# Performance work log

Hardware: AMD Instinct MI355X
Metric: run time of the kernel (lower is better)

## Reference

```python
import jax, jax.numpy as jnp
import numpy as np

B, S, D, H, MEL = 64, 512, 512, 8, 80
HD = D // H  # head dim


def _lstm_cell(x, h, c, w_ih, w_hh, b_ih, b_hh):
    # torch gate order: i, f, g, o
    gates = x @ w_ih.T + h @ w_hh.T + b_ih + b_hh
    i, f, g, o = jnp.split(gates, 4, axis=-1)
    c = jax.nn.sigmoid(f) * c + jax.nn.sigmoid(i) * jnp.tanh(g)
    h = jax.nn.sigmoid(o) * jnp.tanh(c)
    return h, c


def setup_inputs() -> dict:
    key = jax.random.key(0)
    ks = jax.random.split(key, 24)
    s = 0.05
    inp = {"encoder_output": jax.random.normal(ks[0], (B, S, D), jnp.float32)}
    # MultiheadAttention params (torch layout: in_proj [3D, D])
    inp["attn_in_w"] = jax.random.normal(ks[1], (3 * D, D), jnp.float32) * s
    inp["attn_in_b"] = jax.random.normal(ks[2], (3 * D,), jnp.float32) * s
    inp["attn_out_w"] = jax.random.normal(ks[3], (D, D), jnp.float32) * s
    inp["attn_out_b"] = jax.random.normal(ks[4], (D,), jnp.float32) * s
    # LSTM1 (2 layers)
    names = [("l1_w_ih0", (4 * D, D)), ("l1_w_hh0", (4 * D, D)), ("l1_b_ih0", (4 * D,)), ("l1_b_hh0", (4 * D,)),
             ("l1_w_ih1", (4 * D, D)), ("l1_w_hh1", (4 * D, D)), ("l1_b_ih1", (4 * D,)), ("l1_b_hh1", (4 * D,)),
             ("l2_w_ih", (4 * D, D)), ("l2_w_hh", (4 * D, D)), ("l2_b_ih", (4 * D,)), ("l2_b_hh", (4 * D,)),
             ("proj_w", (MEL, D)), ("proj_b", (MEL,))]
    for i, (n, shp) in enumerate(names):
        inp[n] = jax.random.normal(ks[5 + i], shp, jnp.float32) * s
    return inp


def reference(encoder_output, attn_in_w, attn_in_b, attn_out_w, attn_out_b,
              l1_w_ih0, l1_w_hh0, l1_b_ih0, l1_b_hh0,
              l1_w_ih1, l1_w_hh1, l1_b_ih1, l1_b_hh1,
              l2_w_ih, l2_w_hh, l2_b_ih, l2_b_hh, proj_w, proj_b):
    b, s, d = encoder_output.shape
    max_len = s * 5
    wq, wk, wv = jnp.split(attn_in_w, 3, axis=0)
    bq, bk, bv = jnp.split(attn_in_b, 3, axis=0)
    # Precompute K, V over encoder output: [B, S, H, HD]
    K = (encoder_output @ wk.T + bk).reshape(b, s, H, HD)
    V = (encoder_output @ wv.T + bv).reshape(b, s, H, HD)
    scale = 1.0 / np.sqrt(HD)

    def attend(x):  # x: [B, D] single-token query
        q = ((x @ wq.T + bq) * scale).reshape(b, H, HD)
        scores = jnp.einsum('bhd,bshd->bhs', q, K)
        w = jax.nn.softmax(scores, axis=-1)
        ctx = jnp.einsum('bhs,bshd->bhd', w, V).reshape(b, d)
        return ctx @ attn_out_w.T + attn_out_b

    zeros = jnp.zeros((b, d), encoder_output.dtype)
    carry0 = (zeros, zeros, zeros, zeros, zeros, zeros, zeros)

    def step(carry, _):
        h10, c10, h11, c11, h2, c2, dec_in = carry
        h10, c10 = _lstm_cell(dec_in, h10, c10, l1_w_ih0, l1_w_hh0, l1_b_ih0, l1_b_hh0)
        h11, c11 = _lstm_cell(h10, h11, c11, l1_w_ih1, l1_w_hh1, l1_b_ih1, l1_b_hh1)
        attn_out = attend(h11)
        h2, c2 = _lstm_cell(attn_out, h2, c2, l2_w_ih, l2_w_hh, l2_b_ih, l2_b_hh)
        out = h2 @ proj_w.T + proj_b  # [B, MEL]
        return (h10, c10, h11, c11, h2, c2, h2), out

    _, ys = jax.lax.scan(step, carry0, None, length=max_len)
    return jnp.transpose(ys, (1, 0, 2))  # [B, max_len, MEL]
```

## Files before the change

kernel.cpp:

```cpp
#include <hip/hip_runtime.h>
#include <hip/hip_bf16.h>
#include <hip/hip_fp8.h>

#define DEV_INLINE __device__ __forceinline__

typedef __attribute__((ext_vector_type(8))) short bf16x8;
typedef __attribute__((ext_vector_type(4))) float f32x4;
typedef __attribute__((ext_vector_type(2))) float f32x2;
typedef __attribute__((ext_vector_type(4))) unsigned int u32x4;
typedef unsigned long long ull;

constexpr int Bc = 64, Sc = 512, Dc = 512, Hc = 8, HDc = 64, MELc = 80, Tc = 2560;
constexpr int OUTSTRIDE = Tc * MELc;

constexpr size_t SZ_KP8 = 64ull * 8 * 512 * 64;
constexpr size_t SZ_VP  = 64ull * 8 * 512 * 64 * 2;
constexpr size_t SZ_PL  = 128ull * 2048 * 16;
constexpr size_t OFF_KP8 = 0;
constexpr size_t OFF_VP  = OFF_KP8 + SZ_KP8;
constexpr size_t OFF_PL0 = OFF_VP + SZ_VP;
constexpr size_t OFF_PL1 = OFF_PL0 + SZ_PL;
constexpr size_t OFF_PL2 = OFF_PL1 + SZ_PL;
constexpr size_t OFF_PWQ = OFF_PL2 + SZ_PL;
constexpr size_t OFF_PP  = OFF_PWQ + 524288;
constexpr size_t OFF_BL0 = OFF_PP + 81920;
constexpr size_t OFF_BL1 = OFF_BL0 + 8192;
constexpr size_t OFF_BL2 = OFF_BL1 + 8192;
constexpr size_t OFF_B2E = OFF_BL2 + 8192;
constexpr size_t OFF_W2E = OFF_B2E + 8192;
constexpr size_t OFF_WOT = OFF_W2E + 2097152;
constexpr size_t OFF_ACT = OFF_WOT + 1048576;
constexpr size_t OFF_FLG = OFF_ACT + 524288;

constexpr unsigned DYN_LDS = 121088;

DEV_INLINE float bf2f(short s) { return __uint_as_float(((unsigned)(unsigned short)s) << 16); }
DEV_INLINE short f2bf(float f) { union { __hip_bfloat16 h; short s; } u; u.h = __float2bfloat16(f); return u.s; }
DEV_INLINE float sig_f(float x) { return 1.0f / (1.0f + __expf(-x)); }
DEV_INLINE float tanh_f(float x) {
  float ax = fabsf(x);
  float e = __expf(fminf(2.0f * ax, 80.0f));
  float r = 1.0f - 2.0f / (e + 1.0f);
  return copysignf(r, x);
}
DEV_INLINE bf16x8 cvt8(const float* p) {
  bf16x8 r;
#pragma unroll
  for (int i = 0; i < 8; ++i) r[i] = f2bf(p[i]);
  return r;
}
DEV_INLINE float fp8tof(unsigned v) {
  __hip_fp8_e4m3 t; t.__x = (__hip_fp8_storage_t)v; return (float)t;
}

template <bool HI>
DEV_INLINE f32x2 cvt2_fp8(unsigned w) {
#if defined(__has_builtin) && __has_builtin(__builtin_amdgcn_cvt_pk_f32_fp8)
  return __builtin_amdgcn_cvt_pk_f32_fp8(w, HI);
#else
  unsigned b = HI ? (w >> 16) : w;
  f32x2 r; r[0] = fp8tof(b & 0xFFu); r[1] = fp8tof((b >> 8) & 0xFFu);
  return r;
#endif
}

DEV_INLINE ull ld_dev_u64(const void* p) {
  return __hip_atomic_load((const ull*)p, __ATOMIC_RELAXED, __HIP_MEMORY_SCOPE_AGENT);
}
DEV_INLINE void st_dev_u64(void* p, ull v) {
  __hip_atomic_store((ull*)p, v, __ATOMIC_RELAXED, __HIP_MEMORY_SCOPE_AGENT);
}
DEV_INLINE bf16x8 ld_frag(const __hip_bfloat16* p) {
  union { bf16x8 v; ull u[2]; } r;
  r.u[0] = ld_dev_u64(p);
  r.u[1] = ld_dev_u64((const char*)p + 8);
  return r.v;
}

__global__ __launch_bounds__(256) void gemm_setup(const float* __restrict__ A,
                                                  const float* __restrict__ Bt,
                                                  const float* __restrict__ bias,
                                                  __hip_bfloat16* __restrict__ dst,
                                                  unsigned char* __restrict__ dst8,
                                                  int mode) {
  int tid = threadIdx.x, lane = tid & 63, wv = tid >> 6;
  int m0 = blockIdx.y * 64 + wv * 16;
  int nb = blockIdx.x * 64;
  int mrow = m0 + (lane & 15);
  int kb = (lane >> 4) * 8;
  f32x4 acc0 = {0,0,0,0}, acc1 = {0,0,0,0}, acc2 = {0,0,0,0}, acc3 = {0,0,0,0};
  const float* arow = A + (size_t)mrow * 512 + kb;
  const float* b0r = Bt + (size_t)(nb + 0 * 16 + (lane & 15)) * 512 + kb;
  const float* b1r = Bt + (size_t)(nb + 1 * 16 + (lane & 15)) * 512 + kb;
  const float* b2r = Bt + (size_t)(nb + 2 * 16 + (lane & 15)) * 512 + kb;
  const float* b3r = Bt + (size_t)(nb + 3 * 16 + (lane & 15)) * 512 + kb;
  for (int kk = 0; kk < 16; ++kk) {
    bf16x8 af = cvt8(arow + kk * 32);
    acc0 = __builtin_amdgcn_mfma_f32_16x16x32_bf16(af, cvt8(b0r + kk * 32), acc0, 0, 0, 0);
    acc1 = __builtin_amdgcn_mfma_f32_16x16x32_bf16(af, cvt8(b1r + kk * 32), acc1, 0, 0, 0);
    acc2 = __builtin_amdgcn_mfma_f32_16x16x32_bf16(af, cvt8(b2r + kk * 32), acc2, 0, 0, 0);
    acc3 = __builtin_amdgcn_mfma_f32_16x16x32_bf16(af, cvt8(b3r + kk * 32), acc3, 0, 0, 0);
  }
  int col16 = lane & 15, r0 = (lane >> 4) * 4;
  f32x4 accs[4] = {acc0, acc1, acc2, acc3};
#pragma unroll
  for (int nt = 0; nt < 4; ++nt) {
    int n = nb + nt * 16 + col16;
#pragma unroll
    for (int r = 0; r < 4; ++r) {
      int m = m0 + r0 + r;
      float v = accs[nt][r];
      if (mode == 0) {
        v += bias[n];
        int bb = m >> 9, s = m & 511, h = n >> 6, d = n & 63;
        dst[(((size_t)(bb * 8 + h) * 512 + s) * 64) + d] = __float2bfloat16(v);
      } else if (mode == 2) {
        v += bias[n];
        int bb = m >> 9, s = m & 511, h = n >> 6, d = n & 63;
        __hip_fp8_e4m3 q(v);
        dst8[(((size_t)(bb * 8 + h) * 512 + s) * 64) + d] = (unsigned char)q.__x;
      } else {
        dst[(size_t)m * 512 + n] = __float2bfloat16(v);
      }
    }
  }
}

__global__ __launch_bounds__(256) void transpose512(const float* __restrict__ in, float* __restrict__ out) {
  __shared__ float tl[32][33];
  int x = threadIdx.x & 31, ty = threadIdx.x >> 5;
  int bx = blockIdx.x * 32, by = blockIdx.y * 32;
#pragma unroll
  for (int r = 0; r < 4; ++r) tl[ty + r * 8][x] = in[(size_t)(by + ty + r * 8) * 512 + bx + x];
  __syncthreads();
#pragma unroll
  for (int r = 0; r < 4; ++r) out[(size_t)(bx + ty + r * 8) * 512 + by + x] = tl[x][ty + r * 8];
}

__global__ __launch_bounds__(256) void b2eff_k(const float* __restrict__ w2ih, const float* __restrict__ bout,
                                               const float* __restrict__ bih, const float* __restrict__ bhh,
                                               float* __restrict__ dst) {
  int g = blockIdx.x * 256 + threadIdx.x;
  float acc = bih[g] + bhh[g];
  const float* row = w2ih + (size_t)g * 512;
  for (int k = 0; k < 512; ++k) acc += row[k] * bout[k];
  dst[g] = acc;
}

__global__ __launch_bounds__(256) void pack_lstm(const float* __restrict__ lo_f32,
                                                 const __hip_bfloat16* __restrict__ lo_bf16,
                                                 const float* __restrict__ hi_f32,
                                                 const float* __restrict__ b1, const float* __restrict__ b2,
                                                 const float* __restrict__ b_pre,
                                                 __hip_bfloat16* __restrict__ dst, float* __restrict__ bias_out,
                                                 int mode) {
  int u = blockIdx.x, tid = threadIdx.x;
  for (int rep = 0; rep < 8; ++rep) {
    int slot = rep * 256 + tid;
    int kk = slot >> 6, lane = slot & 63;
    int n16 = lane & 15, gate = n16 >> 2, jj = n16 & 3;
    int srow = gate * 512 + u * 4 + jj;
    int k = kk * 32 + (lane >> 4) * 8;
    __hip_bfloat16 tmp[8];
    if (k < 512) {
      if (mode == 0) {
#pragma unroll
        for (int i = 0; i < 8; ++i) tmp[i] = __float2bfloat16(lo_f32[(size_t)srow * 512 + k + i]);
      } else {
#pragma unroll
        for (int i = 0; i < 8; ++i) tmp[i] = lo_bf16[(size_t)srow * 512 + k + i];
      }
    } else {
#pragma unroll
      for (int i = 0; i < 8; ++i) tmp[i] = __float2bfloat16(hi_f32[(size_t)srow * 512 + (k - 512) + i]);
    }
    *(uint4*)(dst + ((size_t)u * 2048 + slot) * 8) = *(uint4*)tmp;
  }
  if (tid < 16) {
    int gate = tid >> 2, jj = tid & 3;
    int srow = gate * 512 + u * 4 + jj;
    bias_out[u * 16 + tid] = (mode == 0) ? (b1[srow] + b2[srow]) : b_pre[srow];
  }
}

__global__ __launch_bounds__(256) void pack_wq(const float* __restrict__ wq, __hip_bfloat16* __restrict__ dst) {
  int h = blockIdx.x, tid = threadIdx.x;
  for (int rep = 0; rep < 16; ++rep) {
    int slot = rep * 256 + tid;
    int nt = slot >> 10, kk = (slot >> 6) & 15, lane = slot & 63;
    int srow = h * 64 + nt * 16 + (lane & 15);
    int k = kk * 32 + (lane >> 4) * 8;
    __hip_bfloat16 tmp[8];
#pragma unroll
    for (int i = 0; i < 8; ++i) tmp[i] = __float2bfloat16(wq[(size_t)srow * 512 + k + i]);
    *(uint4*)(dst + ((size_t)h * 4096 + slot) * 8) = *(uint4*)tmp;
  }
}

struct DecParams {
  const float* attn_in_b;
  const float* proj_b;
  const float* proj_w;
  const uint4* packL0; const uint4* packL1; const uint4* packL2;
  const float* biasL0; const float* biasL1; const float* biasL2;
  const uint4* packWq;
  const unsigned char* Kp8; const __hip_bfloat16* Vp;
  __hip_bfloat16* h10b; __hip_bfloat16* h11b; __hip_bfloat16* h2b; __hip_bfloat16* ctxb;
  ull* actbase;
  unsigned* flags;
  float* out;
};

constexpr ull WD_TICKS = 200000000ull;

DEV_INLINE void publish_flag(unsigned* flags, int wg, unsigned id, int tid) {
  __builtin_amdgcn_s_waitcnt(0);
  __syncthreads();
  if (tid == 0)
    __hip_atomic_store(&flags[wg], id, __ATOMIC_RELAXED, __HIP_MEMORY_SCOPE_AGENT);
}

DEV_INLINE bool wait_flags(unsigned* flags, int base, int count, unsigned id, int tid,
                           ull t0, int* bail) {
  if (tid < 64) {
    for (;;) {
      bool ok = true;
      for (int i = tid; i < count; i += 64)
        ok &= (__hip_atomic_load(&flags[base + i], __ATOMIC_RELAXED, __HIP_MEMORY_SCOPE_AGENT) >= id);
      if (__all(ok ? 1 : 0)) break;
      if (__builtin_amdgcn_s_memrealtime() - t0 > WD_TICKS) { if (tid == 0) *bail = 1; break; }
      __builtin_amdgcn_s_sleep(1);
    }
  }
  __syncthreads();
  if (*bail) return false;
  return true;
}

DEV_INLINE bool wait_half(unsigned* flags, int base, unsigned id, int lane, ull t0, int* sbail) {
  for (;;) {
    unsigned f0 = __hip_atomic_load(&flags[base + lane], __ATOMIC_RELAXED, __HIP_MEMORY_SCOPE_AGENT);
    unsigned f1 = __hip_atomic_load(&flags[base + lane], __ATOMIC_RELAXED, __HIP_MEMORY_SCOPE_AGENT);
    if (__all(f0 >= id ? 1 : 0)) return true;
    if (__all(f1 >= id ? 1 : 0)) return true;
    if (__builtin_amdgcn_s_memrealtime() - t0 > WD_TICKS) { *sbail = 1; return false; }
    __builtin_amdgcn_s_sleep(1);
  }
}

DEV_INLINE void prefetch_hi(bf16x8* pf, const __hip_bfloat16* hi, int g, int lane, int wv) {
  if (wv >= 2) {
    const __hip_bfloat16* p = hi + (size_t)(g * 32 + (wv & 1) * 16 + (lane & 15)) * 512 + (lane >> 4) * 8;
#pragma unroll
    for (int kk = 0; kk < 16; ++kk) pf[kk] = ld_frag(p + kk * 32);
  }
}

DEV_INLINE bool lstm_stage(int tid, int g, int wgl,
                           const uint4* wlds, const float* bias,
                           const __hip_bfloat16* lo, const bf16x8* pf,
                           float* cstate, __hip_bfloat16* hc,
                           float* pred, ull* st64,
                           unsigned* flags, int fbase, unsigned id,
                           ull t0, int* sbail) {
  const int lane = tid & 63, wv = tid >> 6, mt = wv & 1, kh = wv >> 1;
  f32x4 acc = {0,0,0,0};
  if (kh == 0) {
    const __hip_bfloat16* pA = lo + (size_t)(g * 32 + mt * 16 + (lane & 15)) * 512 + (lane >> 4) * 8;
    if (wait_half(flags, fbase, id, lane, t0, sbail)) {
#pragma unroll
      for (int kk = 0; kk < 8; ++kk) {
        bf16x8 a = ld_frag(pA + kk * 32);
        bf16x8 b = *(const bf16x8*)(wlds + kk * 64 + lane);
        acc = __builtin_amdgcn_mfma_f32_16x16x32_bf16(a, b, acc, 0, 0, 0);
      }
      if (wait_half(flags, fbase + 64, id, lane, t0, sbail)) {
#pragma unroll
        for (int kk = 8; kk < 16; ++kk) {
          bf16x8 a = ld_frag(pA + kk * 32);
          bf16x8 b = *(const bf16x8*)(wlds + kk * 64 + lane);
          acc = __builtin_amdgcn_mfma_f32_16x16x32_bf16(a, b, acc, 0, 0, 0);
        }
      }
    }
  } else {
#pragma unroll
    for (int kk = 0; kk < 16; ++kk) {
      bf16x8 b = *(const bf16x8*)(wlds + (16 + kk) * 64 + lane);
      acc = __builtin_amdgcn_mfma_f32_16x16x32_bf16(pf[kk], b, acc, 0, 0, 0);
    }
  }
#pragma unroll
  for (int r = 0; r < 4; ++r) pred[wv * 256 + lane * 4 + r] = acc[r];
  __syncthreads();
  if (*sbail) return false;
  if (tid < 128) {
    int bl = tid >> 2, j = tid & 3;
    int mt2 = bl >> 4, qd = (bl & 15) >> 2, reg = bl & 3;
    const float* p0 = pred + mt2 * 256;
    const float* p1 = pred + (2 + mt2) * 256;
    int l0 = qd * 16;
    float gi = p0[(l0 + j) * 4 + reg]      + p1[(l0 + j) * 4 + reg]      + bias[j];
    float gf = p0[(l0 + 4 + j) * 4 + reg]  + p1[(l0 + 4 + j) * 4 + reg]  + bias[4 + j];
    float gg = p0[(l0 + 8 + j) * 4 + reg]  + p1[(l0 + 8 + j) * 4 + reg]  + bias[8 + j];
    float go = p0[(l0 + 12 + j) * 4 + reg] + p1[(l0 + 12 + j) * 4 + reg] + bias[12 + j];
    float c = cstate[tid & 127];
    c = sig_f(gf) * c + sig_f(gi) * tanh_f(gg);
    float h = sig_f(go) * tanh_f(c);
    cstate[tid & 127] = c;
    ((unsigned short*)st64)[tid] = (unsigned short)f2bf(h);
  }
  __syncthreads();
  if (tid < 32)
    st_dev_u64(hc + (size_t)(g * 32 + tid) * 512 + wgl * 4, st64[tid]);
  return true;
}

DEV_INLINE void proj_spread(int tid, int g, int wgl, const float* pw, const float* pb,
                            const __hip_bfloat16* h2in, float* outp) {
  const int lane = tid & 63, pr = tid >> 6;
#pragma unroll
  for (int r = 0; r < 5; ++r) {
    int P = wgl * 20 + r * 4 + pr;
    int b = P / 80, m = P - b * 80;
    bf16x8 hv = ld_frag(h2in + (size_t)(g * 32 + b) * 512 + lane * 8);
    const f32x4* w4 = (const f32x4*)(pw + (size_t)m * 512 + lane * 8);
    f32x4 wa = w4[0], wb = w4[1];
    float acc = bf2f(hv[0]) * wa[0] + bf2f(hv[1]) * wa[1] + bf2f(hv[2]) * wa[2] + bf2f(hv[3]) * wa[3]
              + bf2f(hv[4]) * wb[0] + bf2f(hv[5]) * wb[1] + bf2f(hv[6]) * wb[2] + bf2f(hv[7]) * wb[3];
#pragma unroll
    for (int off = 32; off; off >>= 1) acc += __shfl_xor(acc, off);
    if (lane == 0) outp[(size_t)(g * 32 + b) * OUTSTRIDE + m] = acc + pb[m];
  }
}

__global__ __launch_bounds__(256, 1) void decoder_main(DecParams P) {
  extern __shared__ char smem[];
  uint4* wL0 = (uint4*)smem;
  uint4* wL1 = wL0 + 2048;
  uint4* wL2 = wL1 + 2048;
  ull*   st64 = (ull*)(wL2 + 2048);
  float* pred = (float*)(st64 + 32);
  float* qls  = pred + 1024;
  float* sco  = qls + 1088;
  float* red  = sco + 1024;
  float* cst  = red + 2048;
  float* smx  = cst + 384;
  float* ssum = smx + 4;
  float* sinv = ssum + 4;
  int*   sbail = (int*)(sinv + 2);

  const int wg = blockIdx.x, tid = threadIdx.x;
  const int lane = tid & 63, wv = tid >> 6;
  const int g = wg >> 7;
  const int wgl = wg & 127;
  const int fbase = g * 128;
  const int hh = wgl >> 4;
  const int b0g = (wgl & 15) * 2;
  const int bblk = b0g & ~15;

  const ull t0 = __builtin_amdgcn_s_memrealtime();

  {
    const uint4* s0 = P.packL0 + (size_t)wgl * 2048;
    const uint4* s1 = P.packL1 + (size_t)wgl * 2048;
    const uint4* s2 = P.packL2 + (size_t)wgl * 2048;
    for (int i = tid; i < 2048; i += 256) { wL0[i] = s0[i]; wL1[i] = s1[i]; wL2[i] = s2[i]; }
  }
  if (tid == 0) *sbail = 0;
  if (tid < 128) { cst[tid] = 0.0f; cst[128 + tid] = 0.0f; cst[256 + tid] = 0.0f; }
  st_dev_u64(P.actbase + (size_t)wg * 256 + tid, 0ull);
  __syncthreads();
  publish_flag(P.flags, wg, 1u, tid);
  if (!wait_flags(P.flags, 0, 256, 1u, tid, t0, sbail)) goto bail;

  for (int t = 0; t < Tc; ++t) {
    const int cur = t & 1, pv = cur ^ 1;
    const unsigned idA = 4u * t + 1, idApub = 4u * t + 2, idBpub = 4u * t + 3,
                   idCpub = 4u * t + 4, idDpub = 4u * t + 5;
    __hip_bfloat16* h10c = P.h10b + cur * 32768; __hip_bfloat16* h10p = P.h10b + pv * 32768;
    __hip_bfloat16* h11c = P.h11b + cur * 32768; __hip_bfloat16* h11p = P.h11b + pv * 32768;
    __hip_bfloat16* h2c  = P.h2b  + cur * 32768; __hip_bfloat16* h2p  = P.h2b  + pv * 32768;
    __hip_bfloat16* ctxc = P.ctxb + cur * 32768;

    {
      bf16x8 pf[16];
      prefetch_hi(pf, h10p, g, lane, wv);
      if (!lstm_stage(tid, g, wgl, wL0, P.biasL0 + wgl * 16, h2p, pf, cst, h10c, pred, st64,
                      P.flags, fbase, idA, t0, sbail)) goto bail;
      publish_flag(P.flags, wg, idApub, tid);
    }
    if (t > 0)
      proj_spread(tid, g, wgl, P.proj_w, P.proj_b, h2p, P.out + (size_t)(t - 1) * MELc);

    {
      bf16x8 pf[16];
      prefetch_hi(pf, h11p, g, lane, wv);
      if (!lstm_stage(tid, g, wgl, wL1, P.biasL1 + wgl * 16, h10c, pf, cst + 128, h11c, pred, st64,
                      P.flags, fbase, idApub, t0, sbail)) goto bail;
      publish_flag(P.flags, wg, idBpub, tid);
    }

    {
      int mrow = g * 32 + bblk + (lane & 15);
      const __hip_bfloat16* pA = h11c + (size_t)mrow * 512 + (lane >> 4) * 8;
      const uint4* pB = P.packWq + (size_t)hh * 4096 + wv * 1024;
      f32x4 acc = {0,0,0,0};
      if (wait_half(P.flags, fbase, idBpub, lane, t0, sbail)) {
#pragma unroll
        for (int kk = 0; kk < 8; ++kk) {
          bf16x8 a = ld_frag(pA + kk * 32);
          bf16x8 b = *(const bf16x8*)(pB + kk * 64 + lane);
          acc = __builtin_amdgcn_mfma_f32_16x16x32_bf16(a, b, acc, 0, 0, 0);
        }
        if (wait_half(P.flags, fbase + 64, idBpub, lane, t0, sbail)) {
#pragma unroll
          for (int kk = 8; kk < 16; ++kk) {
            bf16x8 a = ld_frag(pA + kk * 32);
            bf16x8 b = *(const bf16x8*)(pB + kk * 64 + lane);
            acc = __builtin_amdgcn_mfma_f32_16x16x32_bf16(a, b, acc, 0, 0, 0);
          }
        }
      }
      int col = lane & 15, row0 = (lane >> 4) << 2;
      int dg = wv * 16 + col;
      float bq = P.attn_in_b[hh * 64 + dg];
#pragma unroll
      for (int r = 0; r < 4; ++r) qls[(row0 + r) * 68 + dg] = (acc[r] + bq) * 0.125f;
    }
    __syncthreads();
    if (*sbail) goto bail;
    {
      int p = tid >> 7, si = tid & 127;
      int bg = g * 32 + b0g + p;
      const float* qv = qls + ((b0g & 15) + p) * 68;
      f32x4 q4[16];
#pragma unroll
      for (int i = 0; i < 16; ++i) q4[i] = *(const f32x4*)(qv + 4 * i);
      const u32x4* Kb = (const u32x4*)(P.Kp8 + (size_t)(bg * 8 + hh) * 512 * 64);
#pragma unroll
      for (int ss = 0; ss < 4; ++ss) {
        int s = si * 4 + ss;
        const u32x4* kr = Kb + s * 4;
        f32x2 acc2 = {0.0f, 0.0f};
#pragma unroll
        for (int i = 0; i < 4; ++i) {
          u32x4 kv = kr[i];
#pragma unroll
          for (int j = 0; j < 4; ++j) {
            unsigned w = kv[j];
            f32x2 c01 = cvt2_fp8<false>(w);
            f32x2 c23 = cvt2_fp8<true>(w);
            f32x4 qq = q4[i * 4 + j];
            acc2 += c01 * (f32x2){qq[0], qq[1]} + c23 * (f32x2){qq[2], qq[3]};
          }
        }
        sco[p * 512 + s] = acc2[0] + acc2[1];
      }
    }
    __syncthreads();
    {
      int p = wv >> 1, half = wv & 1;
      int idx = tid & 127;
      float mx = -1e30f;
#pragma unroll
      for (int ss = 0; ss < 4; ++ss) mx = fmaxf(mx, sco[p * 512 + idx * 4 + ss]);
#pragma unroll
      for (int off = 32; off; off >>= 1) mx = fmaxf(mx, __shfl_xor(mx, off));
      if (lane == 0) smx[p * 2 + half] = mx;
      __syncthreads();
      float m = fmaxf(smx[p * 2], smx[p * 2 + 1]);
      float sum = 0.0f;
#pragma unroll
      for (int ss = 0; ss < 4; ++ss) {
        int ix = p * 512 + idx * 4 + ss;
        float e = __expf(sco[ix] - m);
        sco[ix] = e; sum += e;
      }
#pragma unroll
      for (int off = 32; off; off >>= 1) sum += __shfl_xor(sum, off);
      if (lane == 0) ssum[p * 2 + half] = sum;
      __syncthreads();
      if (tid < 2) sinv[tid] = 1.0f / (ssum[tid * 2] + ssum[tid * 2 + 1]);
    }
    __syncthreads();
    {
      int p = wv >> 1, half = wv & 1;
      int bg = g * 32 + b0g + p;
      int sg = lane >> 3, dj = lane & 7;
      const char* Vb = (const char*)(P.Vp + (size_t)(bg * 8 + hh) * 512 * 64);
      f32x2 aA[4] = {{0,0},{0,0},{0,0},{0,0}};
      f32x2 aB[4] = {{0,0},{0,0},{0,0},{0,0}};
      const int s0 = half * 256 + sg;
#pragma unroll 4
      for (int it = 0; it < 16; ++it) {
        int sA = s0 + it * 8, sB = sA + 128;
        const char* pa = Vb + (size_t)sA * 128 + dj * 16;
        const char* pq = Vb + (size_t)sB * 128 + dj * 16;
        ull a0 = ld_dev_u64(pa), a1 = ld_dev_u64(pa + 8);
        ull b0 = ld_dev_u64(pq), b1 = ld_dev_u64(pq + 8);
        float wa = sco[p * 512 + sA], wb = sco[p * 512 + sB];
        f32x2 wA = {wa, wa}, wB = {wb, wb};
        unsigned va[4] = {(unsigned)a0, (unsigned)(a0 >> 32), (unsigned)a1, (unsigned)(a1 >> 32)};
        unsigned vb[4] = {(unsigned)b0, (unsigned)(b0 >> 32), (unsigned)b1, (unsigned)(b1 >> 32)};
#pragma unroll
        for (int j = 0; j < 4; ++j) {
          f32x2 fa = { __uint_as_float(va[j] << 16), __uint_as_float(va[j] & 0xFFFF0000u) };
          f32x2 fb = { __uint_as_float(vb[j] << 16), __uint_as_float(vb[j] & 0xFFFF0000u) };
          aA[j] += wA * fa;
          aB[j] += wB * fb;
        }
      }
      float* rp = red + ((p * 16 + half * 8 + sg) * 64) + dj * 8;
#pragma unroll
      for (int j = 0; j < 4; ++j) {
        rp[j * 2]     = aA[j][0] + aB[j][0];
        rp[j * 2 + 1] = aA[j][1] + aB[j][1];
      }
    }
    __syncthreads();
    if (tid < 128) {
      int p = tid >> 6, d = tid & 63;
      float sacc = 0.0f;
#pragma unroll
      for (int k = 0; k < 16; ++k) sacc += red[(p * 16 + k) * 64 + d];
      sacc *= sinv[p];
      ((unsigned short*)st64)[tid] = (unsigned short)f2bf(sacc);
    }
    __syncthreads();
    if (tid < 32) {
      int p = tid >> 4, q = tid & 15;
      st_dev_u64(ctxc + (size_t)(g * 32 + b0g + p) * 512 + hh * 64 + q * 4, st64[p * 16 + q]);
    }
    publish_flag(P.flags, wg, idCpub, tid);

    {
      bf16x8 pf[16];
      prefetch_hi(pf, h2p, g, lane, wv);
      if (!lstm_stage(tid, g, wgl, wL2, P.biasL2 + wgl * 16, ctxc, pf, cst + 256, h2c, pred, st64,
                      P.flags, fbase, idCpub, t0, sbail)) goto bail;
      publish_flag(P.flags, wg, idDpub, tid);
    }
  }

  if (wait_flags(P.flags, fbase, 128, 4u * (Tc - 1) + 5, tid, t0, sbail))
    proj_spread(tid, g, wgl, P.proj_w, P.proj_b, P.h2b + ((Tc - 1) & 1) * 32768,
                P.out + (size_t)(Tc - 1) * MELc);
  return;

bail:
  publish_flag(P.flags, wg, 0x7F000000u, tid);
}

extern "C" void kernel_launch(void* const* d_in, const int* in_sizes, int n_in,
                              void* d_out, int out_size, void* d_ws, size_t ws_size,
                              hipStream_t stream) {
  const float* enc        = (const float*)d_in[0];
  const float* attn_in_w  = (const float*)d_in[1];
  const float* attn_in_b  = (const float*)d_in[2];
  const float* attn_out_w = (const float*)d_in[3];
  const float* attn_out_b = (const float*)d_in[4];
  const float* w_ih0 = (const float*)d_in[5];
  const float* w_hh0 = (const float*)d_in[6];
  const float* b_ih0 = (const float*)d_in[7];
  const float* b_hh0 = (const float*)d_in[8];
  const float* w_ih1 = (const float*)d_in[9];
  const float* w_hh1 = (const float*)d_in[10];
  const float* b_ih1 = (const float*)d_in[11];
  const float* b_hh1 = (const float*)d_in[12];
  const float* w_ih2 = (const float*)d_in[13];
  const float* w_hh2 = (const float*)d_in[14];
  const float* b_ih2 = (const float*)d_in[15];
  const float* b_hh2 = (const float*)d_in[16];
  const float* proj_w = (const float*)d_in[17];
  const float* proj_b = (const float*)d_in[18];

  char* ws = (char*)d_ws;
  unsigned char*  Kp8 = (unsigned char*)(ws + OFF_KP8);
  __hip_bfloat16* Vp  = (__hip_bfloat16*)(ws + OFF_VP);
  __hip_bfloat16* pl0 = (__hip_bfloat16*)(ws + OFF_PL0);
  __hip_bfloat16* pl1 = (__hip_bfloat16*)(ws + OFF_PL1);
  __hip_bfloat16* pl2 = (__hip_bfloat16*)(ws + OFF_PL2);
  __hip_bfloat16* pwq = (__hip_bfloat16*)(ws + OFF_PWQ);
  float* bl0 = (float*)(ws + OFF_BL0);
  float* bl1 = (float*)(ws + OFF_BL1);
  float* bl2 = (float*)(ws + OFF_BL2);
  float* b2e = (float*)(ws + OFF_B2E);
  __hip_bfloat16* w2e = (__hip_bfloat16*)(ws + OFF_W2E);
  float* wot = (float*)(ws + OFF_WOT);
  char* act  = ws + OFF_ACT;
  unsigned* flags = (unsigned*)(ws + OFF_FLG);

  hipMemsetAsync(flags, 0, 4096, stream);

  gemm_setup<<<dim3(8, 512), 256, 0, stream>>>(enc, attn_in_w + 512 * 512, attn_in_b + 512, nullptr, Kp8, 2);
  gemm_setup<<<dim3(8, 512), 256, 0, stream>>>(enc, attn_in_w + 1024 * 512, attn_in_b + 1024, Vp, nullptr, 0);
  transpose512<<<dim3(16, 16), 256, 0, stream>>>(attn_out_w, wot);
  gemm_setup<<<dim3(8, 32), 256, 0, stream>>>(w_ih2, wot, nullptr, w2e, nullptr, 1);
  b2eff_k<<<8, 256, 0, stream>>>(w_ih2, attn_out_b, b_ih2, b_hh2, b2e);
  pack_lstm<<<128, 256, 0, stream>>>(w_ih0, nullptr, w_hh0, b_ih0, b_hh0, nullptr, pl0, bl0, 0);
  pack_lstm<<<128, 256, 0, stream>>>(w_ih1, nullptr, w_hh1, b_ih1, b_hh1, nullptr, pl1, bl1, 0);
  pack_lstm<<<128, 256, 0, stream>>>(nullptr, w2e, w_hh2, nullptr, nullptr, b2e, pl2, bl2, 1);
  pack_wq<<<8, 256, 0, stream>>>(attn_in_w, pwq);

  DecParams p;
  p.attn_in_b = attn_in_b;
  p.proj_b = proj_b;
  p.proj_w = proj_w;
  p.packL0 = (const uint4*)pl0; p.packL1 = (const uint4*)pl1; p.packL2 = (const uint4*)pl2;
  p.biasL0 = bl0; p.biasL1 = bl1; p.biasL2 = bl2;
  p.packWq = (const uint4*)pwq;
  p.Kp8 = Kp8; p.Vp = Vp;
  p.h10b = (__hip_bfloat16*)(act + 0);
  p.h11b = (__hip_bfloat16*)(act + 131072);
  p.h2b  = (__hip_bfloat16*)(act + 262144);
  p.ctxb = (__hip_bfloat16*)(act + 393216);
  p.actbase = (ull*)act;
  p.flags = flags;
  p.out = (float*)d_out;

  (void)hipFuncSetAttribute((const void*)decoder_main,
                            hipFuncAttributeMaxDynamicSharedMemorySize, DYN_LDS);
  decoder_main<<<dim3(256), dim3(256), DYN_LDS, stream>>>(p);
}
```

Measured before the change: 107.4 ms.

## Replace per-workgroup flag arrays with per-stage atomic counters for inter-WG sync

Each workgroup now signals a stage's completion by atomically incrementing a shared counter per group, stage and half, instead of storing its own flag. Waiters poll a single counter with one scalar load rather than scanning 64 flags per wavefront, which cuts polling traffic and latency on the critical serial path of the 2560-step recurrence. In exchange, all workgroups in a group contend on the same atomic address, and the bail path has to bump every counter to release the others. The V-accumulation loop unroll is also raised from 4 to 8.

Result: no change. 106.0 ms (-1.3%).

```diff
diff --git a/kernel.cpp b/kernel.cpp
--- a/kernel.cpp
+++ b/kernel.cpp
@@ -213,36 +213,22 @@
 
 constexpr ull WD_TICKS = 200000000ull;
 
-DEV_INLINE void publish_flag(unsigned* flags, int wg, unsigned id, int tid) {
+DEV_INLINE unsigned* ctrp(unsigned* f, int g, int s, int h) {
+  return f + 32 + (((g << 2) + s) * 2 + h) * 32;
+}
+
+DEV_INLINE void publish_ctr(unsigned* c, int tid) {
   __builtin_amdgcn_s_waitcnt(0);
   __syncthreads();
   if (tid == 0)
-    __hip_atomic_store(&flags[wg], id, __ATOMIC_RELAXED, __HIP_MEMORY_SCOPE_AGENT);
-}
-
-DEV_INLINE bool wait_flags(unsigned* flags, int base, int count, unsigned id, int tid,
-                           ull t0, int* bail) {
-  if (tid < 64) {
-    for (;;) {
-      bool ok = true;
-      for (int i = tid; i < count; i += 64)
-        ok &= (__hip_atomic_load(&flags[base + i], __ATOMIC_RELAXED, __HIP_MEMORY_SCOPE_AGENT) >= id);
-      if (__all(ok ? 1 : 0)) break;
-      if (__builtin_amdgcn_s_memrealtime() - t0 > WD_TICKS) { if (tid == 0) *bail = 1; break; }
-      __builtin_amdgcn_s_sleep(1);
-    }
-  }
-  __syncthreads();
-  if (*bail) return false;
-  return true;
-}
-
-DEV_INLINE bool wait_half(unsigned* flags, int base, unsigned id, int lane, ull t0, int* sbail) {
+    (void)__hip_atomic_fetch_add(c, 1u, __ATOMIC_RELAXED, __HIP_MEMORY_SCOPE_AGENT);
+}
+
+DEV_INLINE bool wait_ctr(unsigned* c, unsigned target, ull t0, int* sbail) {
   for (;;) {
-    unsigned f0 = __hip_atomic_load(&flags[base + lane], __ATOMIC_RELAXED, __HIP_MEMORY_SCOPE_AGENT);
-    unsigned f1 = __hip_atomic_load(&flags[base + lane], __ATOMIC_RELAXED, __HIP_MEMORY_SCOPE_AGENT);
-    if (__all(f0 >= id ? 1 : 0)) return true;
-    if (__all(f1 >= id ? 1 : 0)) return true;
+    unsigned v = (unsigned)__builtin_amdgcn_readfirstlane(
+        (int)__hip_atomic_load(c, __ATOMIC_RELAXED, __HIP_MEMORY_SCOPE_AGENT));
+    if (v >= target) return true;
     if (__builtin_amdgcn_s_memrealtime() - t0 > WD_TICKS) { *sbail = 1; return false; }
     __builtin_amdgcn_s_sleep(1);
   }
@@ -261,20 +247,20 @@
                            const __hip_bfloat16* lo, const bf16x8* pf,
                            float* cstate, __hip_bfloat16* hc,
                            float* pred, ull* st64,
-                           unsigned* flags, int fbase, unsigned id,
+                           unsigned* c_lo, unsigned* c_hi, unsigned target,
                            ull t0, int* sbail) {
   const int lane = tid & 63, wv = tid >> 6, mt = wv & 1, kh = wv >> 1;
   f32x4 acc = {0,0,0,0};
   if (kh == 0) {
     const __hip_bfloat16* pA = lo + (size_t)(g * 32 + mt * 16 + (lane & 15)) * 512 + (lane >> 4) * 8;
-    if (wait_half(flags, fbase, id, lane, t0, sbail)) {
+    if (wait_ctr(c_lo, target, t0, sbail)) {
 #pragma unroll
       for (int kk = 0; kk < 8; ++kk) {
         bf16x8 a = ld_frag(pA + kk * 32);
         bf16x8 b = *(const bf16x8*)(wlds + kk * 64 + lane);
         acc = __builtin_amdgcn_mfma_f32_16x16x32_bf16(a, b, acc, 0, 0, 0);
       }
-      if (wait_half(flags, fbase + 64, id, lane, t0, sbail)) {
+      if (wait_ctr(c_hi, target, t0, sbail)) {
 #pragma unroll
         for (int kk = 8; kk < 16; ++kk) {
           bf16x8 a = ld_frag(pA + kk * 32);
@@ -354,12 +340,13 @@
   const int lane = tid & 63, wv = tid >> 6;
   const int g = wg >> 7;
   const int wgl = wg & 127;
-  const int fbase = g * 128;
+  const int myhalf = wgl >> 6;
   const int hh = wgl >> 4;
   const int b0g = (wgl & 15) * 2;
   const int bblk = b0g & ~15;
 
   const ull t0 = __builtin_amdgcn_s_memrealtime();
+  unsigned* F = P.flags;
 
   {
     const uint4* s0 = P.packL0 + (size_t)wgl * 2048;
@@ -371,13 +358,14 @@
   if (tid < 128) { cst[tid] = 0.0f; cst[128 + tid] = 0.0f; cst[256 + tid] = 0.0f; }
   st_dev_u64(P.actbase + (size_t)wg * 256 + tid, 0ull);
   __syncthreads();
-  publish_flag(P.flags, wg, 1u, tid);
-  if (!wait_flags(P.flags, 0, 256, 1u, tid, t0, sbail)) goto bail;
+  publish_ctr(F, tid);
+  if (!wait_ctr(F, 256u, t0, sbail)) goto bail;
+  __syncthreads();
 
   for (int t = 0; t < Tc; ++t) {
     const int cur = t & 1, pv = cur ^ 1;
-    const unsigned idA = 4u * t + 1, idApub = 4u * t + 2, idBpub = 4u * t + 3,
-                   idCpub = 4u * t + 4, idDpub = 4u * t + 5;
+    const unsigned tgtP = 64u * (unsigned)t;
+    const unsigned tgtC = 64u * (unsigned)(t + 1);
     __hip_bfloat16* h10c = P.h10b + cur * 32768; __hip_bfloat16* h10p = P.h10b + pv * 32768;
     __hip_bfloat16* h11c = P.h11b + cur * 32768; __hip_bfloat16* h11p = P.h11b + pv * 32768;
     __hip_bfloat16* h2c  = P.h2b  + cur * 32768; __hip_bfloat16* h2p  = P.h2b  + pv * 32768;
@@ -387,8 +375,8 @@
       bf16x8 pf[16];
       prefetch_hi(pf, h10p, g, lane, wv);
       if (!lstm_stage(tid, g, wgl, wL0, P.biasL0 + wgl * 16, h2p, pf, cst, h10c, pred, st64,
-                      P.flags, fbase, idA, t0, sbail)) goto bail;
-      publish_flag(P.flags, wg, idApub, tid);
+                      ctrp(F, g, 3, 0), ctrp(F, g, 3, 1), tgtP, t0, sbail)) goto bail;
+      publish_ctr(ctrp(F, g, 0, myhalf), tid);
     }
     if (t > 0)
       proj_spread(tid, g, wgl, P.proj_w, P.proj_b, h2p, P.out + (size_t)(t - 1) * MELc);
@@ -397,8 +385,8 @@
       bf16x8 pf[16];
       prefetch_hi(pf, h11p, g, lane, wv);
       if (!lstm_stage(tid, g, wgl, wL1, P.biasL1 + wgl * 16, h10c, pf, cst + 128, h11c, pred, st64,
-                      P.flags, fbase, idApub, t0, sbail)) goto bail;
-      publish_flag(P.flags, wg, idBpub, tid);
+                      ctrp(F, g, 0, 0), ctrp(F, g, 0, 1), tgtC, t0, sbail)) goto bail;
+      publish_ctr(ctrp(F, g, 1, myhalf), tid);
     }
 
     {
@@ -406,14 +394,14 @@
       const __hip_bfloat16* pA = h11c + (size_t)mrow * 512 + (lane >> 4) * 8;
       const uint4* pB = P.packWq + (size_t)hh * 4096 + wv * 1024;
       f32x4 acc = {0,0,0,0};
-      if (wait_half(P.flags, fbase, idBpub, lane, t0, sbail)) {
+      if (wait_ctr(ctrp(F, g, 1, 0), tgtC, t0, sbail)) {
 #pragma unroll
         for (int kk = 0; kk < 8; ++kk) {
           bf16x8 a = ld_frag(pA + kk * 32);
           bf16x8 b = *(const bf16x8*)(pB + kk * 64 + lane);
           acc = __builtin_amdgcn_mfma_f32_16x16x32_bf16(a, b, acc, 0, 0, 0);
         }
-        if (wait_half(P.flags, fbase + 64, idBpub, lane, t0, sbail)) {
+        if (wait_ctr(ctrp(F, g, 1, 1), tgtC, t0, sbail)) {
 #pragma unroll
           for (int kk = 8; kk < 16; ++kk) {
             bf16x8 a = ld_frag(pA + kk * 32);
@@ -492,7 +480,7 @@
       f32x2 aA[4] = {{0,0},{0,0},{0,0},{0,0}};
       f32x2 aB[4] = {{0,0},{0,0},{0,0},{0,0}};
       const int s0 = half * 256 + sg;
-#pragma unroll 4
+#pragma unroll 8
       for (int it = 0; it < 16; ++it) {
         int sA = s0 + it * 8, sB = sA + 128;
         const char* pa = Vb + (size_t)sA * 128 + dj * 16;
@@ -532,24 +520,34 @@
       int p = tid >> 4, q = tid & 15;
       st_dev_u64(ctxc + (size_t)(g * 32 + b0g + p) * 512 + hh * 64 + q * 4, st64[p * 16 + q]);
     }
-    publish_flag(P.flags, wg, idCpub, tid);
+    publish_ctr(ctrp(F, g, 2, myhalf), tid);
 
     {
       bf16x8 pf[16];
       prefetch_hi(pf, h2p, g, lane, wv);
       if (!lstm_stage(tid, g, wgl, wL2, P.biasL2 + wgl * 16, ctxc, pf, cst + 256, h2c, pred, st64,
-                      P.flags, fbase, idCpub, t0, sbail)) goto bail;
-      publish_flag(P.flags, wg, idDpub, tid);
-    }
-  }
-
-  if (wait_flags(P.flags, fbase, 128, 4u * (Tc - 1) + 5, tid, t0, sbail))
+                      ctrp(F, g, 2, 0), ctrp(F, g, 2, 1), tgtC, t0, sbail)) goto bail;
+      publish_ctr(ctrp(F, g, 3, myhalf), tid);
+    }
+  }
+
+  if (wait_ctr(ctrp(F, g, 3, 0), 64u * Tc, t0, sbail) &&
+      wait_ctr(ctrp(F, g, 3, 1), 64u * Tc, t0, sbail)) {
+    __syncthreads();
     proj_spread(tid, g, wgl, P.proj_w, P.proj_b, P.h2b + ((Tc - 1) & 1) * 32768,
                 P.out + (size_t)(Tc - 1) * MELc);
+  }
   return;
 
 bail:
-  publish_flag(P.flags, wg, 0x7F000000u, tid);
+  if (tid == 0) {
+    (void)__hip_atomic_fetch_add(F, 1u << 20, __ATOMIC_RELAXED, __HIP_MEMORY_SCOPE_AGENT);
+    for (int gg = 0; gg < 2; ++gg)
+      for (int s = 0; s < 4; ++s)
+        for (int h = 0; h < 2; ++h)
+          (void)__hip_atomic_fetch_add(ctrp(F, gg, s, h), 1u << 20,
+                                       __ATOMIC_RELAXED, __HIP_MEMORY_SCOPE_AGENT);
+  }
 }
 
 extern "C" void kernel_launch(void* const* d_in, const int* in_sizes, int n_in,
```
